# Kernel optimization log

Hardware: AMD Instinct MI355X
Metric: run time of the kernel (lower is better)

Reference implementation:

```python
import jax, jax.numpy as jnp
import numpy as np

GRID_SIZE = 5
SPLINE_ORDER = 3
INPUT_DIM = 4096
BATCH = 4096
N_BASIS = GRID_SIZE + SPLINE_ORDER - 1  # 7


def _extended_knots():
    # Uniform grid on [-1, 1] extended by spline_order knots on each side so the
    # Cox-de Boor recursion is well defined (the original torch code indexes
    # grid[i+k+1] past the end; this is the standard intended knot extension).
    grid = np.linspace(-1.0, 1.0, GRID_SIZE)
    h = grid[1] - grid[0]
    left = grid[0] - h * np.arange(SPLINE_ORDER, 0, -1)
    right = grid[-1] + h * np.arange(1, SPLINE_ORDER + 1)
    return jnp.asarray(np.concatenate([left, grid, right]), dtype=jnp.float32)  # (11,)


def _bspline_basis(x, knots):
    # x: (B, D) -> basis: (B, D, N_BASIS), fully vectorized Cox-de Boor recursion.
    t = knots
    xe = x[..., None]                                   # (B, D, 1)
    Bk = ((xe >= t[:-1]) & (xe < t[1:])).astype(x.dtype)  # degree 0: (B, D, 10)
    for k in range(1, SPLINE_ORDER + 1):
        n = t.shape[0] - k - 1
        left = (xe - t[:n]) / (t[k:k + n] - t[:n]) * Bk[..., :n]
        right = (t[k + 1:k + 1 + n] - xe) / (t[k + 1:k + 1 + n] - t[1:1 + n]) * Bk[..., 1:n + 1]
        Bk = left + right
    return Bk  # (B, D, 7)


def setup_inputs() -> dict:
    key = jax.random.key(0)
    kx, kc = jax.random.split(key)
    x = jax.random.uniform(kx, (BATCH, INPUT_DIM), dtype=jnp.float32, minval=-1.0, maxval=1.0)
    coeffs = jax.random.normal(kc, (INPUT_DIM, N_BASIS), dtype=jnp.float32)
    return {"x": x, "coeffs": coeffs}


def reference(x, coeffs):
    knots = _extended_knots()
    basis = _bspline_basis(x, knots)          # (B, D, K)
    return jnp.einsum('bdk,dk->bd', basis, coeffs)
```

## Files before the change

### kernel.cpp

```cpp
#include <hip/hip_runtime.h>


#define INPUT_DIM 4096
#define BATCH     4096
#define N_BASIS   7

constexpr int N_ELEM = BATCH * INPUT_DIM;
constexpr int N_VEC4 = N_ELEM / 4;

__global__ __launch_bounds__(256) void
spline_act_kernel(const float* __restrict__ x,
                  const float* __restrict__ coeffs,
                  float* __restrict__ out) {
    int t = blockIdx.x * blockDim.x + threadIdx.x;
    if (t >= N_VEC4) return;

    const float4* x4 = reinterpret_cast<const float4*>(x);
    float4*       o4 = reinterpret_cast<float4*>(out);

    float4 xv = x4[t];
    int d0 = (t * 4) & (INPUT_DIM - 1);

    float xs[4] = {xv.x, xv.y, xv.z, xv.w};
    float r[4];

#pragma unroll
    for (int j = 0; j < 4; ++j) {
        float u = (xs[j] + 1.0f) * 2.0f;
        int c = (int)floorf(u);
        c = c < 0 ? 0 : (c > 3 ? 3 : c);
        float s = u - (float)c;

        float s2 = s * s;
        float s3 = s2 * s;
        float omt = 1.0f - s;
        const float k6 = 1.0f / 6.0f;
        float w0 = omt * omt * omt * k6;
        float w1 = (3.0f * s3 - 6.0f * s2 + 4.0f) * k6;
        float w2 = (-3.0f * s3 + 3.0f * s2 + 3.0f * s + 1.0f) * k6;
        float w3 = s3 * k6;

        const float* cp = coeffs + (d0 + j) * N_BASIS + c;
        r[j] = w0 * cp[0] + w1 * cp[1] + w2 * cp[2] + w3 * cp[3];
    }

    o4[t] = make_float4(r[0], r[1], r[2], r[3]);
}

extern "C" void kernel_launch(void* const* d_in, const int* in_sizes, int n_in,
                              void* d_out, int out_size, void* d_ws, size_t ws_size,
                              hipStream_t stream) {
    const float* x      = (const float*)d_in[0];
    const float* coeffs = (const float*)d_in[1];
    float* out          = (float*)d_out;

    const int block = 256;
    const int grid  = (N_VEC4 + block - 1) / block;
    spline_act_kernel<<<grid, block, 0, stream>>>(x, coeffs, out);
}
```

Baseline: 131.8 us.

## Stage per-tile spline coefficients in LDS and process multiple rows per block

Each block now owns a 512-column tile and 16 rows. It first copies that tile's 512x7 coefficients into shared memory, then each thread handles 8 rows, reading coefficients from LDS instead of doing scattered global gathers. This aims to cut redundant, uncoalesced coefficient traffic through the cache hierarchy. The costs are a staging load and barrier per block, possible LDS bank conflicts from the stride-7 indexing, and fewer blocks in the grid.

```diff
diff --git a/kernel.cpp b/kernel.cpp
--- a/kernel.cpp
+++ b/kernel.cpp
@@ -1,50 +1,72 @@
 #include <hip/hip_runtime.h>
 
 
-#define INPUT_DIM 4096
-#define BATCH     4096
-#define N_BASIS   7
+#define D       4096
+#define B       4096
+#define NB      7
+#define DTILE   512
+#define ROWS    16
 
-constexpr int N_ELEM = BATCH * INPUT_DIM;
-constexpr int N_VEC4 = N_ELEM / 4;
+constexpr int NDT   = D / DTILE;
+constexpr int NRT   = B / ROWS;
+constexpr int NCOEF = DTILE * NB;
 
-__global__ __launch_bounds__(256) void
+__global__ __launch_bounds__(256, 8) void
 spline_act_kernel(const float* __restrict__ x,
                   const float* __restrict__ coeffs,
                   float* __restrict__ out) {
-    int t = blockIdx.x * blockDim.x + threadIdx.x;
-    if (t >= N_VEC4) return;
+    __shared__ float sc[NCOEF];
+
+    const int bid   = blockIdx.x;
+    const int dt    = bid & (NDT - 1);
+    const int rowt  = bid >> 3;
+    const int dbase = dt * DTILE;
+
+    for (int i = threadIdx.x; i < NCOEF; i += 256)
+        sc[i] = coeffs[dbase * NB + i];
+    __syncthreads();
+
+    const int tid  = threadIdx.x;
+    const int pos  = tid & 127;
+    const int rsub = tid >> 7;
+    const int dl0  = pos * 4;
 
     const float4* x4 = reinterpret_cast<const float4*>(x);
     float4*       o4 = reinterpret_cast<float4*>(out);
 
-    float4 xv = x4[t];
-    int d0 = (t * 4) & (INPUT_DIM - 1);
+    const int rowbase = rowt * ROWS;
+    const float k6 = 1.0f / 6.0f;
 
-    float xs[4] = {xv.x, xv.y, xv.z, xv.w};
-    float r[4];
+#pragma unroll 2
+    for (int it = 0; it < ROWS / 2; ++it) {
+        int row = rowbase + it * 2 + rsub;
+        int idx = row * (D / 4) + (dbase >> 2) + pos;
+
+        float4 xv = x4[idx];
+        float xs[4] = {xv.x, xv.y, xv.z, xv.w};
+        float r[4];
 
 #pragma unroll
-    for (int j = 0; j < 4; ++j) {
-        float u = (xs[j] + 1.0f) * 2.0f;
-        int c = (int)floorf(u);
-        c = c < 0 ? 0 : (c > 3 ? 3 : c);
-        float s = u - (float)c;
+        for (int j = 0; j < 4; ++j) {
+            float u = (xs[j] + 1.0f) * 2.0f;
+            int c = (int)floorf(u);
+            c = c < 0 ? 0 : (c > 3 ? 3 : c);
+            float s = u - (float)c;
 
-        float s2 = s * s;
-        float s3 = s2 * s;
-        float omt = 1.0f - s;
-        const float k6 = 1.0f / 6.0f;
-        float w0 = omt * omt * omt * k6;
-        float w1 = (3.0f * s3 - 6.0f * s2 + 4.0f) * k6;
-        float w2 = (-3.0f * s3 + 3.0f * s2 + 3.0f * s + 1.0f) * k6;
-        float w3 = s3 * k6;
+            float s2  = s * s;
+            float s3  = s2 * s;
+            float omt = 1.0f - s;
+            float w0 = omt * omt * omt * k6;
+            float w1 = (3.0f * s3 - 6.0f * s2 + 4.0f) * k6;
+            float w2 = (-3.0f * s3 + 3.0f * s2 + 3.0f * s + 1.0f) * k6;
+            float w3 = s3 * k6;
 
-        const float* cp = coeffs + (d0 + j) * N_BASIS + c;
-        r[j] = w0 * cp[0] + w1 * cp[1] + w2 * cp[2] + w3 * cp[3];
+            const float* cp = &sc[(dl0 + j) * NB + c];
+            r[j] = w0 * cp[0] + w1 * cp[1] + w2 * cp[2] + w3 * cp[3];
+        }
+
+        o4[idx] = make_float4(r[0], r[1], r[2], r[3]);
     }
-
-    o4[t] = make_float4(r[0], r[1], r[2], r[3]);
 }
 
 extern "C" void kernel_launch(void* const* d_in, const int* in_sizes, int n_in,
@@ -54,7 +76,6 @@
     const float* coeffs = (const float*)d_in[1];
     float* out          = (float*)d_out;
 
-    const int block = 256;
-    const int grid  = (N_VEC4 + block - 1) / block;
-    spline_act_kernel<<<grid, block, 0, stream>>>(x, coeffs, out);
+    const int grid = NDT * NRT;
+    spline_act_kernel<<<grid, 256, 0, stream>>>(x, coeffs, out);
 }
```

After: 115.6 us. 1.14x faster.
